# Kernel optimization log

Hardware: AMD Instinct MI355X
Metric: run time of the kernel (lower is better)

The kernel has to match this reference:

```python
import jax, jax.numpy as jnp
import numpy as np

B, N, D = 2, 2048, 1024
H, DH = 16, 64  # heads, dim_head; dim_hidden = H*DH = 1024


def setup_inputs() -> dict:
    key = jax.random.key(0)
    ks = jax.random.split(key, 5)
    s = 0.02
    return {
        "x": jax.random.normal(ks[0], (B, N, D), dtype=jnp.float32),
        "W_w": jax.random.normal(ks[1], (3 * H * DH, D), dtype=jnp.float32) * s,
        "W_b": jax.random.normal(ks[2], (3 * H * DH,), dtype=jnp.float32) * s,
        "out_w": jax.random.normal(ks[3], (D, H * DH), dtype=jnp.float32) * s,
        "out_b": jax.random.normal(ks[4], (D,), dtype=jnp.float32) * s,
    }


def reference(x, W_w, W_b, out_w, out_b):
    b, n, _ = x.shape
    qkv = x @ W_w.T + W_b                       # [b, n, 3*H*DH]
    Q, K, V = jnp.split(qkv, 3, axis=-1)
    split_heads = lambda t: t.reshape(b, n, H, DH).transpose(0, 2, 1, 3)  # [b,h,n,dh]
    q, k, v = map(split_heads, (Q, K, V))
    scale = DH ** -0.5
    dots = jnp.einsum('bhik,bhjk->bhij', q, k) * scale   # [b,h,n,n]
    attn = jax.nn.softmax(dots, axis=-1)
    out = jnp.einsum('bhij,bhjk->bhik', attn, v)         # [b,h,n,dh]
    out = out.transpose(0, 2, 1, 3).reshape(b, n, H * DH)
    return out @ out_w.T + out_b
```

## Files before the change

### kernel.cpp

```cpp
#include <hip/hip_runtime.h>
#include <hip/hip_bf16.h>
#include <stdint.h>

#define BB 2
#define NN 2048
#define DD 1024
#define HH 16
#define DHD 64
#define MTOT (BB*NN)
#define QKVC (3*HH*DHD)

typedef unsigned short u16;
typedef __attribute__((ext_vector_type(8))) short short8;
typedef __attribute__((ext_vector_type(4))) float f32x4;
typedef __attribute__((ext_vector_type(16))) float f32x16;

#define QSCALE (0.125f * 1.44269504088896f)

#if __has_builtin(__builtin_amdgcn_exp2f)
#define EXP2(x) __builtin_amdgcn_exp2f(x)
#else
#define EXP2(x) exp2f(x)
#endif

static __device__ __forceinline__ u16 f2bf(float f) {
  union { float f; uint32_t u; } v; v.f = f;
  uint32_t r = (v.u + 0x7fffu + ((v.u >> 16) & 1u)) >> 16;
  return (u16)r;
}

static __device__ __forceinline__ uint32_t cvtpk_bf16(float lo, float hi) {
  uint32_t r;
  asm("v_cvt_pk_bf16_f32 %0, %1, %2" : "=v"(r) : "v"(lo), "v"(hi));
  return r;
}

static __device__ __forceinline__ float u2f(uint32_t u) {
  union { uint32_t u; float f; } v; v.u = u; return v.f;
}
static __device__ __forceinline__ uint32_t f2u(float f) {
  union { float f; uint32_t u; } v; v.f = f; return v.u;
}

static __device__ __forceinline__ void gload_lds16(const void* g, void* l) {
  __builtin_amdgcn_global_load_lds(
      (const __attribute__((address_space(1))) void*)g,
      (__attribute__((address_space(3))) void*)l, 16, 0, 0);
}

#define MFMA16(a, b, c) __builtin_amdgcn_mfma_f32_16x16x32_bf16((a), (b), (c), 0, 0, 0)
#define MFMA32(a, b, c) __builtin_amdgcn_mfma_f32_32x32x16_bf16((a), (b), (c), 0, 0, 0)

__global__ void k_cvt_all(const float* __restrict__ x, const float* __restrict__ Ww,
                          const float* __restrict__ ow,
                          u16* __restrict__ xb, u16* __restrict__ wwb, u16* __restrict__ owb) {
  int i = blockIdx.x * blockDim.x + threadIdx.x;
  const float* src; u16* dst; int off;
  if (i < 1048576)      { src = x;  dst = xb;  off = i; }
  else if (i < 1835008) { src = Ww; dst = wwb; off = i - 1048576; }
  else                  { src = ow; dst = owb; off = i - 1835008; }
  float4 v = ((const float4*)src)[off];
  ushort4 o;
  o.x = f2bf(v.x); o.y = f2bf(v.y); o.z = f2bf(v.z); o.w = f2bf(v.w);
  ((ushort4*)dst)[off] = o;
}

template<int EPI, int BM, int BN>
__global__ __launch_bounds__(256, EPI ? 4 : 3) void k_gemm_bt(
    const u16* __restrict__ A,
    const u16* __restrict__ Bm,
    const float* __restrict__ bias,
    u16* __restrict__ Qo, u16* __restrict__ Ko, u16* __restrict__ Vt,
    float* __restrict__ Co,
    int M, int NC, int K)
{
  constexpr int WM = BM / 2, WN = BN / 2;
  constexpr int FM = WM / 16, FN = WN / 16;
  __shared__ alignas(16) u16 As[2][BM * 32];
  __shared__ alignas(16) u16 Bs[2][BN * 32];
  const int t = threadIdx.x;
  const int lane = t & 63;
  const int wid = t >> 6;
  const int wr = wid >> 1, wc = wid & 1;
  const int l16 = lane & 15, lg = lane >> 4;
  const int col0 = blockIdx.x * BN;
  const int row0 = blockIdx.y * BM;

  f32x4 acc[FM][FN];
#pragma unroll
  for (int i = 0; i < FM; ++i)
#pragma unroll
    for (int j = 0; j < FN; ++j) acc[i][j] = (f32x4){0.f, 0.f, 0.f, 0.f};

  auto stage = [&](int buf, int tt) {
    const int kk = tt * 32;
#pragma unroll
    for (int i = 0; i < BM / 64; ++i) {
      int s = i * 256 + t;
      int r = s >> 2, c8 = (s & 3) * 8;
      gload_lds16(A + (size_t)(row0 + r) * K + kk + c8, ((char*)&As[buf][0]) + s * 16);
    }
#pragma unroll
    for (int i = 0; i < BN / 64; ++i) {
      int s = i * 256 + t;
      int r = s >> 2, c8 = (s & 3) * 8;
      gload_lds16(Bm + (size_t)(col0 + r) * K + kk + c8, ((char*)&Bs[buf][0]) + s * 16);
    }
  };

  auto compute = [&](int buf) {
    const u16* as = &As[buf][0];
    const u16* bs = &Bs[buf][0];
    short8 af[FM], bfr[FN];
#pragma unroll
    for (int i = 0; i < FM; ++i)
      af[i] = *(const short8*)&as[(wr * WM + i * 16 + l16) * 32 + lg * 8];
#pragma unroll
    for (int j = 0; j < FN; ++j)
      bfr[j] = *(const short8*)&bs[(wc * WN + j * 16 + l16) * 32 + lg * 8];
#pragma unroll
    for (int i = 0; i < FM; ++i)
#pragma unroll
      for (int j = 0; j < FN; ++j)
        acc[i][j] = MFMA16(af[i], bfr[j], acc[i][j]);
  };

  const int NT = K / 32;
  stage(0, 0);
  __syncthreads();
  int cur = 0;
  for (int tt = 0; tt < NT; ++tt) {
    if (tt + 1 < NT) stage(cur ^ 1, tt + 1);
    compute(cur);
    __syncthreads();
    cur ^= 1;
  }

  if (EPI == 1) {
#pragma unroll
    for (int j = 0; j < FN; ++j) {
      int col = col0 + wc * WN + j * 16 + l16;
      float bv = bias[col];
#pragma unroll
      for (int i = 0; i < FM; ++i) {
#pragma unroll
        for (int r = 0; r < 4; ++r) {
          int row = row0 + wr * WM + i * 16 + lg * 4 + r;
          Co[(size_t)row * NC + col] = acc[i][j][r] + bv;
        }
      }
    }
  } else {
#pragma unroll
    for (int j = 0; j < FN; ++j) {
      int col = col0 + wc * WN + j * 16 + l16;
      float bv = bias[col];
      int part = col >> 10, rem = col & 1023;
      int h = rem >> 6, dh = rem & 63;
#pragma unroll
      for (int i = 0; i < FM; ++i) {
        int rowb = row0 + wr * WM + i * 16 + lg * 4;
        int b = rowb >> 11;
        int nn = rowb & 2047;
        size_t bhN = (size_t)(b * HH + h) * NN;
        if (part == 0) {
#pragma unroll
          for (int r = 0; r < 4; ++r)
            Qo[(bhN + nn + r) * DHD + dh] = f2bf((acc[i][j][r] + bv) * QSCALE);
        } else if (part == 1) {
#pragma unroll
          for (int r = 0; r < 4; ++r) Ko[(bhN + nn + r) * DHD + dh] = f2bf(acc[i][j][r] + bv);
        } else {
          size_t base = ((size_t)(b * HH + h) * DHD + dh) * NN + nn;
          ushort4 pk;
          pk.x = f2bf(acc[i][j][0] + bv);
          pk.y = f2bf(acc[i][j][1] + bv);
          pk.z = f2bf(acc[i][j][2] + bv);
          pk.w = f2bf(acc[i][j][3] + bv);
          *(ushort4*)&Vt[base] = pk;
        }
      }
    }
  }
}

__global__ __launch_bounds__(256, 4) void k_gemm64(
    const u16* __restrict__ A,
    const u16* __restrict__ Bm,
    const float* __restrict__ bias, float* __restrict__ Co,
    int M, int NC, int K)
{
  __shared__ alignas(16) u16 As[2][64 * 64];
  __shared__ alignas(16) u16 Bs[2][64 * 64];
  const int t = threadIdx.x, lane = t & 63, wid = t >> 6;
  const int wr = wid >> 1, wc = wid & 1;
  const int l16 = lane & 15, lg = lane >> 4;
  const int col0 = blockIdx.x * 64, row0 = blockIdx.y * 64;

  f32x4 acc[2][2];
#pragma unroll
  for (int i = 0; i < 2; ++i)
#pragma unroll
    for (int j = 0; j < 2; ++j) acc[i][j] = (f32x4){0.f, 0.f, 0.f, 0.f};

  auto stage = [&](int buf, int tt) {
    const int kk = tt * 64;
#pragma unroll
    for (int i = 0; i < 2; ++i) {
      int s = i * 256 + t;
      int r = s >> 3, so = ((s & 7) * 16) ^ ((r & 7) << 4);
      gload_lds16((const char*)(A + (size_t)(row0 + r) * K + kk) + so,
                  ((char*)&As[buf][0]) + s * 16);
    }
#pragma unroll
    for (int i = 0; i < 2; ++i) {
      int s = i * 256 + t;
      int r = s >> 3, so = ((s & 7) * 16) ^ ((r & 7) << 4);
      gload_lds16((const char*)(Bm + (size_t)(col0 + r) * K + kk) + so,
                  ((char*)&Bs[buf][0]) + s * 16);
    }
  };

  auto compute = [&](int buf) {
    const char* as = (const char*)&As[buf][0];
    const char* bs = (const char*)&Bs[buf][0];
#pragma unroll
    for (int kkh = 0; kkh < 2; ++kkh) {
      short8 af[2], bfr[2];
#pragma unroll
      for (int i = 0; i < 2; ++i) {
        int row = wr * 32 + i * 16 + l16;
        af[i] = *(const short8*)(as + row * 128 + ((kkh * 64 + lg * 16) ^ ((row & 7) << 4)));
      }
#pragma unroll
      for (int j = 0; j < 2; ++j) {
        int row = wc * 32 + j * 16 + l16;
        bfr[j] = *(const short8*)(bs + row * 128 + ((kkh * 64 + lg * 16) ^ ((row & 7) << 4)));
      }
#pragma unroll
      for (int i = 0; i < 2; ++i)
#pragma unroll
        for (int j = 0; j < 2; ++j)
          acc[i][j] = MFMA16(af[i], bfr[j], acc[i][j]);
    }
  };

  const int NT = K / 64;
  stage(0, 0);
  __syncthreads();
  int cur = 0;
  for (int tt = 0; tt < NT; ++tt) {
    if (tt + 1 < NT) stage(cur ^ 1, tt + 1);
    compute(cur);
    __syncthreads();
    cur ^= 1;
  }

#pragma unroll
  for (int j = 0; j < 2; ++j) {
    int col = col0 + wc * 32 + j * 16 + l16;
    float bv = bias[col];
#pragma unroll
    for (int i = 0; i < 2; ++i)
#pragma unroll
      for (int r = 0; r < 4; ++r) {
        int row = row0 + wr * 32 + i * 16 + lg * 4 + r;
        Co[(size_t)row * NC + col] = acc[i][j][r] + bv;
      }
  }
}

__global__ __launch_bounds__(512, 4) void k_attn(
    const u16* __restrict__ Q, const u16* __restrict__ Kb,
    const u16* __restrict__ Vt, u16* __restrict__ AO)
{
  __shared__ alignas(16) char smem[65536];
  const int t = threadIdx.x, lane = t & 63, w = t >> 6;
  const int g = w >> 2, wg = w & 3;
  const int l32 = lane & 31, hi = lane >> 5;
  const int bid = blockIdx.x;
  const int xcd = bid & 7;
  const int idx = bid >> 3;
  const int bh = xcd * 4 + (idx >> 4);
  const int qt = idx & 15;
  const int b = bh >> 4, h = bh & 15;

  const u16* Qp  = Q + (size_t)bh * NN * DHD;
  const char* Kp = (const char*)(Kb + (size_t)bh * NN * DHD);
  const char* Vp = (const char*)(Vt + (size_t)bh * DHD * NN);

  const int q0 = qt * 128 + wg * 32;

  short8 qf[4];
#pragma unroll
  for (int kk = 0; kk < 4; ++kk)
    qf[kk] = *(const short8*)&Qp[(size_t)(q0 + l32) * DHD + kk * 16 + hi * 8];

  f32x16 oacc[2];
  oacc[0] = (f32x16)(0.f);
  oacc[1] = (f32x16)(0.f);
  float lsv[4] = {0.f, 0.f, 0.f, 0.f};

  char* gbase = smem + g * 32768;
  const int kvbase = g * 1024;

  const int srow = lane >> 3;
  const int scolb = (lane & 7) * 16;
  auto stage = [&](int buf, int kv) {
    char* base = gbase + buf * 16384;
#pragma unroll
    for (int i = 0; i < 2; ++i) {
      int r = wg * 16 + i * 8 + srow;
      gload_lds16(Kp + (size_t)(kv + r) * 128 + (scolb ^ ((r & 7) << 4)),
                  base + wg * 2048 + i * 1024 + lane * 16);
    }
#pragma unroll
    for (int i = 0; i < 2; ++i) {
      int r = wg * 16 + i * 8 + srow;
      gload_lds16(Vp + (size_t)r * (NN * 2) + (size_t)kv * 2 + (scolb ^ ((r & 7) << 4)),
                  base + 8192 + wg * 2048 + i * 1024 + lane * 16);
    }
  };

  auto subtile = [&](const char* bufK, const char* bufV, int sub) {
    const int krow = sub * 32 + l32;
    const char* kro = bufK + krow * 128;
    const int ksw = (krow & 7) << 4;
    short8 kf[4];
#pragma unroll
    for (int kk = 0; kk < 4; ++kk)
      kf[kk] = *(const short8*)(kro + ((kk * 32 + hi * 16) ^ ksw));

    f32x16 s = (f32x16)(0.f);
    __builtin_amdgcn_s_setprio(1);
#pragma unroll
    for (int kk = 0; kk < 4; ++kk) s = MFMA32(kf[kk], qf[kk], s);
    __builtin_amdgcn_s_setprio(0);

    float p[16];
#pragma unroll
    for (int r = 0; r < 16; ++r) p[r] = EXP2(s[r]);
#pragma unroll
    for (int r = 0; r < 16; ++r) lsv[r & 3] += p[r];

#pragma unroll
    for (int gs = 0; gs < 2; ++gs) {
      const int bix = gs * 8;
      uint32_t lo01 = cvtpk_bf16(p[bix + 0], p[bix + 1]);
      uint32_t lo23 = cvtpk_bf16(p[bix + 2], p[bix + 3]);
      uint32_t hi01 = cvtpk_bf16(p[bix + 4], p[bix + 5]);
      uint32_t hi23 = cvtpk_bf16(p[bix + 6], p[bix + 7]);
      auto ra = __builtin_amdgcn_permlane32_swap(lo01, hi01, false, false);
      auto rb = __builtin_amdgcn_permlane32_swap(lo23, hi23, false, false);
      union { uint32_t u[4]; short8 v; } pf;
      pf.u[0] = ra[0]; pf.u[1] = rb[0]; pf.u[2] = ra[1]; pf.u[3] = rb[1];
      __builtin_amdgcn_s_setprio(1);
#pragma unroll
      for (int d = 0; d < 2; ++d) {
        const int vrow = d * 32 + l32;
        short8 vf = *(const short8*)(bufV + vrow * 128 +
                      ((sub * 64 + gs * 32 + hi * 16) ^ ((vrow & 7) << 4)));
        oacc[d] = MFMA32(vf, pf.v, oacc[d]);
      }
      __builtin_amdgcn_s_setprio(0);
    }
  };

  const int NT = 16;
  stage(0, kvbase);
  asm volatile("s_waitcnt vmcnt(0)");
  __syncthreads();
  for (int t2 = 0; t2 < NT; ++t2) {
    int cur = t2 & 1;
    if (t2 + 1 < NT) stage(cur ^ 1, kvbase + (t2 + 1) * 64);
    const char* bK = gbase + cur * 16384;
    const char* bV = bK + 8192;
    subtile(bK, bV, 0);
    subtile(bK, bV, 1);
    asm volatile("s_waitcnt vmcnt(0)");
    __syncthreads();
  }

  float ls = (lsv[0] + lsv[1]) + (lsv[2] + lsv[3]);
  {
    auto rr = __builtin_amdgcn_permlane32_swap(f2u(ls), f2u(ls), false, false);
    ls = u2f(rr[0]) + u2f(rr[1]);
  }
  float* lsarea = (float*)smem;
  float* oarea  = (float*)(smem + 32768);
  if (g == 1) {
    lsarea[wg * 64 + lane] = ls;
    float* dst = oarea + (size_t)(wg * 64 + lane) * 32;
#pragma unroll
    for (int d = 0; d < 2; ++d)
#pragma unroll
      for (int i = 0; i < 4; ++i)
        ((f32x4*)dst)[d * 4 + i] = (f32x4){oacc[d][i*4+0], oacc[d][i*4+1],
                                           oacc[d][i*4+2], oacc[d][i*4+3]};
  }
  __syncthreads();
  if (g == 1) return;

  float lst = ls + lsarea[wg * 64 + lane];
  {
    const float* src = oarea + (size_t)(wg * 64 + lane) * 32;
#pragma unroll
    for (int d = 0; d < 2; ++d)
#pragma unroll
      for (int i = 0; i < 4; ++i) {
        f32x4 v = ((const f32x4*)src)[d * 4 + i];
        oacc[d][i*4+0] += v[0]; oacc[d][i*4+1] += v[1];
        oacc[d][i*4+2] += v[2]; oacc[d][i*4+3] += v[3];
      }
  }

  u16* olw = (u16*)(smem + 1024) + (size_t)wg * 32 * 72;
  float inv = 1.0f / lst;
#pragma unroll
  for (int d = 0; d < 2; ++d) {
#pragma unroll
    for (int i = 0; i < 8; ++i) {
      int r0 = 2 * i;
      int dh = d * 32 + (r0 & 3) + 8 * (r0 >> 2) + 4 * hi;
      uint32_t pk = cvtpk_bf16(oacc[d][r0] * inv, oacc[d][r0 + 1] * inv);
      *(uint32_t*)&olw[l32 * 72 + dh] = pk;
    }
  }
  __builtin_amdgcn_s_waitcnt(0);
#pragma unroll
  for (int rr = 0; rr < 4; ++rr) {
    int row = rr * 8 + (lane >> 3);
    short8 v = *(const short8*)&olw[row * 72 + (lane & 7) * 8];
    int n = q0 + row;
    *(short8*)&AO[((size_t)b * NN + n) * DD + h * DHD + (lane & 7) * 8] = v;
  }
}

extern "C" void kernel_launch(void* const* d_in, const int* in_sizes, int n_in,
                              void* d_out, int out_size, void* d_ws, size_t ws_size,
                              hipStream_t stream) {
  const float* x  = (const float*)d_in[0];
  const float* Ww = (const float*)d_in[1];
  const float* Wb = (const float*)d_in[2];
  const float* ow = (const float*)d_in[3];
  const float* ob = (const float*)d_in[4];
  float* out = (float*)d_out;

  char* ws = (char*)d_ws;
  u16* xb  = (u16*)(ws);
  u16* wwb = (u16*)(ws + ((size_t)8  << 20));
  u16* owb = (u16*)(ws + ((size_t)14 << 20));
  u16* Qb  = (u16*)(ws + ((size_t)16 << 20));
  u16* Kb  = (u16*)(ws + ((size_t)24 << 20));
  u16* Vt  = (u16*)(ws + ((size_t)32 << 20));
  u16* AO  = (u16*)(ws + ((size_t)40 << 20));

  k_cvt_all<<<8192, 256, 0, stream>>>(x, Ww, ow, xb, wwb, owb);

  dim3 g1(QKVC / 128, MTOT / 128);
  k_gemm_bt<0, 128, 128><<<g1, 256, 0, stream>>>(xb, wwb, Wb, Qb, Kb, Vt, nullptr, MTOT, QKVC, DD);

  k_attn<<<512, 512, 0, stream>>>(Qb, Kb, Vt, AO);

  dim3 g3(DD / 64, MTOT / 64);
  k_gemm64<<<g3, 256, 0, stream>>>(AO, owb, ob, out, MTOT, DD, DD);
}
```

Before: 109.2 us.

## Prefetch two K-tiles ahead in GEMMs with vmcnt waits; drop setprio in attention

Both projection GEMM kernels now stage two tiles up front and, after computing a buffer, refill it with the tile two steps ahead. Each iteration waits with s_waitcnt vmcnt(4) before a raw barrier, so global loads get a full compute step to land instead of being waited on right away. The attention kernel's s_setprio calls around the MFMA blocks are removed. The fixed vmcnt count assumes each stage issues exactly four loads; if it doesn't, the wait is either too strict or races.

```diff
diff --git a/kernel.cpp b/kernel.cpp
--- a/kernel.cpp
+++ b/kernel.cpp
@@ -127,13 +127,14 @@
 
   const int NT = K / 32;
   stage(0, 0);
-  __syncthreads();
-  int cur = 0;
+  stage(1, 1);
   for (int tt = 0; tt < NT; ++tt) {
-    if (tt + 1 < NT) stage(cur ^ 1, tt + 1);
-    compute(cur);
-    __syncthreads();
-    cur ^= 1;
+    if (tt == NT - 1) asm volatile("s_waitcnt vmcnt(0)" ::: "memory");
+    else              asm volatile("s_waitcnt vmcnt(4)" ::: "memory");
+    __builtin_amdgcn_s_barrier();
+    compute(tt & 1);
+    __builtin_amdgcn_s_barrier();
+    if (tt + 2 < NT) stage(tt & 1, tt + 2);
   }
 
   if (EPI == 1) {
@@ -247,13 +248,14 @@
 
   const int NT = K / 64;
   stage(0, 0);
-  __syncthreads();
-  int cur = 0;
+  stage(1, 1);
   for (int tt = 0; tt < NT; ++tt) {
-    if (tt + 1 < NT) stage(cur ^ 1, tt + 1);
-    compute(cur);
-    __syncthreads();
-    cur ^= 1;
+    if (tt == NT - 1) asm volatile("s_waitcnt vmcnt(0)" ::: "memory");
+    else              asm volatile("s_waitcnt vmcnt(4)" ::: "memory");
+    __builtin_amdgcn_s_barrier();
+    compute(tt & 1);
+    __builtin_amdgcn_s_barrier();
+    if (tt + 2 < NT) stage(tt & 1, tt + 2);
   }
 
 #pragma unroll
@@ -332,10 +334,8 @@
       kf[kk] = *(const short8*)(kro + ((kk * 32 + hi * 16) ^ ksw));
 
     f32x16 s = (f32x16)(0.f);
-    __builtin_amdgcn_s_setprio(1);
 #pragma unroll
     for (int kk = 0; kk < 4; ++kk) s = MFMA32(kf[kk], qf[kk], s);
-    __builtin_amdgcn_s_setprio(0);
 
     float p[16];
 #pragma unroll
@@ -354,7 +354,6 @@
       auto rb = __builtin_amdgcn_permlane32_swap(lo23, hi23, false, false);
       union { uint32_t u[4]; short8 v; } pf;
       pf.u[0] = ra[0]; pf.u[1] = rb[0]; pf.u[2] = ra[1]; pf.u[3] = rb[1];
-      __builtin_amdgcn_s_setprio(1);
 #pragma unroll
       for (int d = 0; d < 2; ++d) {
         const int vrow = d * 32 + l32;
@@ -362,7 +361,6 @@
                       ((sub * 64 + gs * 32 + hi * 16) ^ ((vrow & 7) << 4)));
         oacc[d] = MFMA32(vf, pf.v, oacc[d]);
       }
-      __builtin_amdgcn_s_setprio(0);
     }
   };
 
```

New measurement: 108.8 us. About the same (-0.4%).

## Single-buffer attention K/V staging to halve LDS and raise occupancy

Applied to the files above, without the earlier changes.

The attention kernel drops double-buffered K/V staging and uses one 16 KB buffer per wave group, so LDS per block falls from 64 KB to about 33 KB. Launch bounds rise from 4 to 8 blocks per CU to exploit the lower footprint. The loads are no longer prefetched, so each step now waits on its loads and pays an extra barrier, and the code counts on more resident blocks to hide that latency. The s_setprio hints are removed and the output-combine area is laid out again, with an added barrier before the bf16 write-back.

```diff
diff --git a/kernel.cpp b/kernel.cpp
--- a/kernel.cpp
+++ b/kernel.cpp
@@ -270,11 +270,11 @@
   }
 }
 
-__global__ __launch_bounds__(512, 4) void k_attn(
+__global__ __launch_bounds__(512, 8) void k_attn(
     const u16* __restrict__ Q, const u16* __restrict__ Kb,
     const u16* __restrict__ Vt, u16* __restrict__ AO)
 {
-  __shared__ alignas(16) char smem[65536];
+  __shared__ alignas(16) char smem[33792];
   const int t = threadIdx.x, lane = t & 63, w = t >> 6;
   const int g = w >> 2, wg = w & 3;
   const int l32 = lane & 31, hi = lane >> 5;
@@ -301,28 +301,29 @@
   oacc[1] = (f32x16)(0.f);
   float lsv[4] = {0.f, 0.f, 0.f, 0.f};
 
-  char* gbase = smem + g * 32768;
+  char* gbase = smem + g * 16384;
   const int kvbase = g * 1024;
 
   const int srow = lane >> 3;
   const int scolb = (lane & 7) * 16;
-  auto stage = [&](int buf, int kv) {
-    char* base = gbase + buf * 16384;
+  auto stage = [&](int kv) {
 #pragma unroll
     for (int i = 0; i < 2; ++i) {
       int r = wg * 16 + i * 8 + srow;
       gload_lds16(Kp + (size_t)(kv + r) * 128 + (scolb ^ ((r & 7) << 4)),
-                  base + wg * 2048 + i * 1024 + lane * 16);
+                  gbase + wg * 2048 + i * 1024 + lane * 16);
     }
 #pragma unroll
     for (int i = 0; i < 2; ++i) {
       int r = wg * 16 + i * 8 + srow;
       gload_lds16(Vp + (size_t)r * (NN * 2) + (size_t)kv * 2 + (scolb ^ ((r & 7) << 4)),
-                  base + 8192 + wg * 2048 + i * 1024 + lane * 16);
-    }
-  };
-
-  auto subtile = [&](const char* bufK, const char* bufV, int sub) {
+                  gbase + 8192 + wg * 2048 + i * 1024 + lane * 16);
+    }
+  };
+
+  auto subtile = [&](int sub) {
+    const char* bufK = gbase;
+    const char* bufV = gbase + 8192;
     const int krow = sub * 32 + l32;
     const char* kro = bufK + krow * 128;
     const int ksw = (krow & 7) << 4;
@@ -332,10 +333,8 @@
       kf[kk] = *(const short8*)(kro + ((kk * 32 + hi * 16) ^ ksw));
 
     f32x16 s = (f32x16)(0.f);
-    __builtin_amdgcn_s_setprio(1);
 #pragma unroll
     for (int kk = 0; kk < 4; ++kk) s = MFMA32(kf[kk], qf[kk], s);
-    __builtin_amdgcn_s_setprio(0);
 
     float p[16];
 #pragma unroll
@@ -354,7 +353,6 @@
       auto rb = __builtin_amdgcn_permlane32_swap(lo23, hi23, false, false);
       union { uint32_t u[4]; short8 v; } pf;
       pf.u[0] = ra[0]; pf.u[1] = rb[0]; pf.u[2] = ra[1]; pf.u[3] = rb[1];
-      __builtin_amdgcn_s_setprio(1);
 #pragma unroll
       for (int d = 0; d < 2; ++d) {
         const int vrow = d * 32 + l32;
@@ -362,22 +360,15 @@
                       ((sub * 64 + gs * 32 + hi * 16) ^ ((vrow & 7) << 4)));
         oacc[d] = MFMA32(vf, pf.v, oacc[d]);
       }
-      __builtin_amdgcn_s_setprio(0);
-    }
-  };
-
-  const int NT = 16;
-  stage(0, kvbase);
-  asm volatile("s_waitcnt vmcnt(0)");
-  __syncthreads();
-  for (int t2 = 0; t2 < NT; ++t2) {
-    int cur = t2 & 1;
-    if (t2 + 1 < NT) stage(cur ^ 1, kvbase + (t2 + 1) * 64);
-    const char* bK = gbase + cur * 16384;
-    const char* bV = bK + 8192;
-    subtile(bK, bV, 0);
-    subtile(bK, bV, 1);
+    }
+  };
+
+  for (int t2 = 0; t2 < 16; ++t2) {
+    stage(kvbase + t2 * 64);
     asm volatile("s_waitcnt vmcnt(0)");
+    __syncthreads();
+    subtile(0);
+    subtile(1);
     __syncthreads();
   }
 
@@ -386,8 +377,8 @@
     auto rr = __builtin_amdgcn_permlane32_swap(f2u(ls), f2u(ls), false, false);
     ls = u2f(rr[0]) + u2f(rr[1]);
   }
-  float* lsarea = (float*)smem;
-  float* oarea  = (float*)(smem + 32768);
+  float* oarea  = (float*)smem;
+  float* lsarea = (float*)(smem + 32768);
   if (g == 1) {
     lsarea[wg * 64 + lane] = ls;
     float* dst = oarea + (size_t)(wg * 64 + lane) * 32;
@@ -399,10 +390,9 @@
                                            oacc[d][i*4+2], oacc[d][i*4+3]};
   }
   __syncthreads();
-  if (g == 1) return;
-
-  float lst = ls + lsarea[wg * 64 + lane];
-  {
+  float lst = 0.f;
+  if (g == 0) {
+    lst = ls + lsarea[wg * 64 + lane];
     const float* src = oarea + (size_t)(wg * 64 + lane) * 32;
 #pragma unroll
     for (int d = 0; d < 2; ++d)
@@ -413,26 +403,29 @@
         oacc[d][i*4+2] += v[2]; oacc[d][i*4+3] += v[3];
       }
   }
-
-  u16* olw = (u16*)(smem + 1024) + (size_t)wg * 32 * 72;
-  float inv = 1.0f / lst;
-#pragma unroll
-  for (int d = 0; d < 2; ++d) {
-#pragma unroll
-    for (int i = 0; i < 8; ++i) {
-      int r0 = 2 * i;
-      int dh = d * 32 + (r0 & 3) + 8 * (r0 >> 2) + 4 * hi;
-      uint32_t pk = cvtpk_bf16(oacc[d][r0] * inv, oacc[d][r0 + 1] * inv);
-      *(uint32_t*)&olw[l32 * 72 + dh] = pk;
-    }
-  }
-  __builtin_amdgcn_s_waitcnt(0);
-#pragma unroll
-  for (int rr = 0; rr < 4; ++rr) {
-    int row = rr * 8 + (lane >> 3);
-    short8 v = *(const short8*)&olw[row * 72 + (lane & 7) * 8];
-    int n = q0 + row;
-    *(short8*)&AO[((size_t)b * NN + n) * DD + h * DHD + (lane & 7) * 8] = v;
+  __syncthreads();
+
+  if (g == 0) {
+    u16* olw = (u16*)smem + (size_t)wg * 32 * 72;
+    float inv = 1.0f / lst;
+#pragma unroll
+    for (int d = 0; d < 2; ++d) {
+#pragma unroll
+      for (int i = 0; i < 8; ++i) {
+        int r0 = 2 * i;
+        int dh = d * 32 + (r0 & 3) + 8 * (r0 >> 2) + 4 * hi;
+        uint32_t pk = cvtpk_bf16(oacc[d][r0] * inv, oacc[d][r0 + 1] * inv);
+        *(uint32_t*)&olw[l32 * 72 + dh] = pk;
+      }
+    }
+    __builtin_amdgcn_s_waitcnt(0);
+#pragma unroll
+    for (int rr = 0; rr < 4; ++rr) {
+      int row = rr * 8 + (lane >> 3);
+      short8 v = *(const short8*)&olw[row * 72 + (lane & 7) * 8];
+      int n = q0 + row;
+      *(short8*)&AO[((size_t)b * NN + n) * DD + h * DHD + (lane & 7) * 8] = v;
+    }
   }
 }
 
```

Measured after the change: 337.4 us. 209% more time.
